# Performance work log

Measured on AMD Instinct MI355X. Metric: run time of the kernel, lower is better.

The kernel has to match this reference:

```python
import jax, jax.numpy as jnp
import numpy as np

QMIN, QMAX = -128.0, 127.0
SMALL_SCALE_THRESHOLD = 6.1e-05


def quant_kernel(x):
    # x: [M, K] float32 -> per-row scale (f32), zero point (i32), precomputed sum (i32), q (i8)
    rmin = jnp.minimum(jnp.min(x, axis=1), 0.0).astype(jnp.float32)
    rmax = jnp.maximum(jnp.max(x, axis=1), 0.0).astype(jnp.float32)
    scale = (rmax - rmin) / (QMAX - QMIN)
    # faithful replication of `scale == 0.0 + isinf(1/scale)` (precedence: 0.0 + bool)
    isinf = jnp.isinf(1.0 / scale)
    scale = jnp.where(scale == (0.0 + isinf.astype(jnp.float32)), 0.1, scale)
    small = scale < SMALL_SCALE_THRESHOLD
    amp = SMALL_SCALE_THRESHOLD / scale
    scale = jnp.where(small, SMALL_SCALE_THRESHOLD, scale)
    rmax = jnp.where(small, amp * rmax, rmax)
    rmin = jnp.where(small, amp * rmin, rmin)
    zp_from_min = QMIN - rmin / scale
    zp_from_max = QMAX - rmax / scale
    err_min = abs(QMIN) + jnp.abs(rmin / scale)
    err_max = abs(QMAX) + jnp.abs(rmax / scale)
    zp0 = jnp.where(err_min < err_max, zp_from_min, zp_from_max)
    zp = jnp.round(zp0).astype(jnp.int32)
    zp = jnp.where(zp0 < QMIN, jnp.int32(QMIN), zp)
    zp = jnp.where(zp0 > QMAX, jnp.int32(QMAX), zp)
    inv = 1.0 / scale
    sums = jnp.round(jnp.sum(x, axis=1) * inv).astype(jnp.int32)
    t = jnp.round(x * inv[:, None]) + zp[:, None].astype(jnp.float32)
    q = jnp.clip(t, QMIN, QMAX).astype(jnp.int8)
    return scale, zp, sums, q


def dequant_kernel(d, bias, m1_scales, m1_zeros, m1_sums, m2_scales, m2_zeros, m2_sums):
    # d: [M, N] int32 raw GEMM; m1_*: [M, 1]; m2_*: [1, N]
    temp = (m1_zeros * m2_sums).astype(jnp.int32) + (m1_sums * m2_zeros).astype(jnp.int32)
    scale = m1_scales * m2_scales
    return bias + ((d - temp).astype(jnp.float32) * scale).astype(bias.dtype)


def setup_inputs() -> dict:
    key = jax.random.key(0)
    k1, k2, k3, k4, k5 = jax.random.split(key, 5)
    B, S, K, N = 4, 4096, 1024, 1024
    inp = jax.random.normal(k1, (B, S, K), dtype=jnp.float32)
    qweight = jax.random.randint(k2, (N, K), -128, 128, dtype=jnp.int32).astype(jnp.int8)
    bias = jax.random.normal(k3, (N,), dtype=jnp.float32)
    w_scales = (jax.random.uniform(k4, (N,), dtype=jnp.float32) * 0.01 + 1e-3)
    w_zeros = jax.random.randint(k5, (N,), -10, 10, dtype=jnp.int32)
    # consistent precomputed weight sums (sum of quantized vals minus K*zero)
    w_sums = (jnp.sum(qweight.astype(jnp.int32), axis=1) - K * w_zeros).astype(jnp.int32)
    return {"inp": inp, "qweight": qweight, "bias": bias,
            "w_scales": w_scales, "w_zeros": w_zeros, "w_sums": w_sums}


def reference(inp, qweight, bias, w_scales, w_zeros, w_sums):
    B, S, K = inp.shape
    x = inp.reshape(B * S, K)
    scales, zeros, sums, qinp = quant_kernel(x)
    # int8 GEMM accumulated in int32: [M, K] @ [K, N]
    d = jnp.matmul(qinp.astype(jnp.int32), qweight.T.astype(jnp.int32))
    M, N = d.shape
    out = dequant_kernel(d, bias, scales.reshape(M, 1), zeros.reshape(M, 1),
                         sums.reshape(M, 1), w_scales.reshape(1, N),
                         w_zeros.reshape(1, N), w_sums.reshape(1, N))
    return out.reshape(B, S, N)
```

## Files before the change

### kernel.cpp

```cpp
#include <hip/hip_runtime.h>
#include <cstdint>
#include <cstddef>

typedef int v4i __attribute__((ext_vector_type(4)));

#define QMIN_F (-128.0f)
#define QMAX_F (127.0f)
#define SMALL_THR 6.1e-05f

#define WAITVM(n) asm volatile("s_waitcnt vmcnt(" #n ")" ::: "memory")
#define WAITLGKM0 asm volatile("s_waitcnt lgkmcnt(0)" ::: "memory")

__global__ __launch_bounds__(256) void quant_rows_kernel(
    const float* __restrict__ x, signed char* __restrict__ q,
    float* __restrict__ scales, int* __restrict__ zps, int* __restrict__ sums,
    const int* __restrict__ w32, int* __restrict__ w8pk, int n4, int K) {
  const int gidx = blockIdx.x * 256 + threadIdx.x;
  if (gidx < n4) {
    v4i pv = *(const v4i*)(w32 + gidx * 4);
    w8pk[gidx] = (pv.x & 255) | ((pv.y & 255) << 8) | ((pv.z & 255) << 16) |
                 (pv.w << 24);
  }

  const int wave = threadIdx.x >> 6;
  const int lane = threadIdx.x & 63;
  const int row  = blockIdx.x * 4 + wave;
  const float* xr = x + (size_t)row * K;

  float4 v[4];
  float vmin = 0.0f, vmax = 0.0f, vsum = 0.0f;
#pragma unroll
  for (int j = 0; j < 4; ++j) {
    v[j] = *(const float4*)(xr + j * 256 + lane * 4);
    vmin = fminf(vmin, fminf(fminf(v[j].x, v[j].y), fminf(v[j].z, v[j].w)));
    vmax = fmaxf(vmax, fmaxf(fmaxf(v[j].x, v[j].y), fmaxf(v[j].z, v[j].w)));
    vsum += (v[j].x + v[j].y) + (v[j].z + v[j].w);
  }
#pragma unroll
  for (int off = 32; off >= 1; off >>= 1) {
    vmin = fminf(vmin, __shfl_xor(vmin, off));
    vmax = fmaxf(vmax, __shfl_xor(vmax, off));
    vsum += __shfl_xor(vsum, off);
  }

  float scale = (vmax - vmin) / (QMAX_F - QMIN_F);
  float isinf_f = isinf(1.0f / scale) ? 1.0f : 0.0f;
  if (scale == isinf_f) scale = 0.1f;
  float rmin = vmin, rmax = vmax;
  if (scale < SMALL_THR) {
    float amp = SMALL_THR / scale;
    scale = SMALL_THR;
    rmax *= amp;
    rmin *= amp;
  }
  float rdmin = rmin / scale, rdmax = rmax / scale;
  float err_min = 128.0f + fabsf(rdmin);
  float err_max = 127.0f + fabsf(rdmax);
  float zp0 = (err_min < err_max) ? (QMIN_F - rdmin) : (QMAX_F - rdmax);
  int zp = (int)rintf(zp0);
  if (zp0 < QMIN_F) zp = -128;
  if (zp0 > QMAX_F) zp = 127;
  float inv = 1.0f / scale;

  if (lane == 0) {
    scales[row] = scale;
    zps[row]    = zp;
    sums[row]   = (int)rintf(vsum * inv);
  }

  const float zpf = (float)zp;
  int* qi = (int*)(q + (size_t)row * K);
#pragma unroll
  for (int j = 0; j < 4; ++j) {
    float t0 = fminf(fmaxf(rintf(v[j].x * inv) + zpf, QMIN_F), QMAX_F);
    float t1 = fminf(fmaxf(rintf(v[j].y * inv) + zpf, QMIN_F), QMAX_F);
    float t2 = fminf(fmaxf(rintf(v[j].z * inv) + zpf, QMIN_F), QMAX_F);
    float t3 = fminf(fmaxf(rintf(v[j].w * inv) + zpf, QMIN_F), QMAX_F);
    int pack = ((int)t0 & 255) | (((int)t1 & 255) << 8) |
               (((int)t2 & 255) << 16) | ((int)t3 << 24);
    qi[j * 64 + lane] = pack;
  }
}

__device__ __forceinline__ void gload_lds16(const void* g, void* l) {
  __builtin_amdgcn_global_load_lds(
      (const __attribute__((address_space(1))) void*)g,
      (__attribute__((address_space(3))) void*)l, 16, 0, 0);
}

__device__ __forceinline__ void stage_tile(
    const signed char* __restrict__ q, const signed char* __restrict__ w,
    char* buf, int rowA0, int rowB0, int k0, int K, int tid) {
#pragma unroll
  for (int i = 0; i < 2; ++i) {
    int c  = (i << 8) + tid;
    int r  = c >> 2;
    int sl = (c & 3) ^ ((r >> 1) & 3);
    gload_lds16(q + (size_t)(rowA0 + r) * K + k0 + (sl << 4), buf + (c << 4));
  }
#pragma unroll
  for (int i = 0; i < 2; ++i) {
    int c  = (i << 8) + tid;
    int r  = c >> 2;
    int sl = (c & 3) ^ ((r >> 1) & 3);
    gload_lds16(w + (size_t)(rowB0 + r) * K + k0 + (sl << 4),
                buf + 8192 + (c << 4));
  }
}

__global__ __launch_bounds__(256, 4) void gemm_dequant_kernel(
    const signed char* __restrict__ q, const signed char* __restrict__ w,
    const float* __restrict__ scales, const int* __restrict__ zps,
    const int* __restrict__ sums, const float* __restrict__ bias,
    const float* __restrict__ w_scales, const int* __restrict__ w_zeros,
    const int* __restrict__ w_sums, float* __restrict__ out,
    int N, int K, int nblk) {
  __shared__ char sh[2][16384];
  const int tid  = threadIdx.x;
  const int lane = tid & 63;
  const int wave = tid >> 6;
  const int wr = wave >> 1;
  const int wc = wave & 1;
  const int fr = lane & 15;
  const int kb = lane >> 4;
  const int ntN = N >> 7;
  const int per = nblk >> 3;
  const int lin = ((int)blockIdx.x & 7) * per + ((int)blockIdx.x >> 3);
  const int rowA0 = (lin / ntN) << 7;
  const int rowB0 = (lin % ntN) << 7;
  const int wrbase = wr << 6;
  const int wcbase = wc << 6;

  v4i acc[4][4];
#pragma unroll
  for (int i = 0; i < 4; ++i)
#pragma unroll
    for (int j = 0; j < 4; ++j) {
      v4i z = {0, 0, 0, 0};
      acc[i][j] = z;
    }

  const int NT = K >> 6;
  stage_tile(q, w, sh[0], rowA0, rowB0, 0, K, tid);

  for (int t = 0; t < NT; ++t) {
    if (t + 1 < NT) {
      stage_tile(q, w, sh[(t + 1) & 1], rowA0, rowB0, (t + 1) << 6, K, tid);
      WAITVM(4);
    } else {
      WAITVM(0);
    }
    __builtin_amdgcn_s_barrier();

    const char* bA = sh[t & 1];
    const char* bB = bA + 8192;

    v4i afrag[4], bfrag[4];
#pragma unroll
    for (int n = 0; n < 4; ++n) {
      int rb = wcbase + (n << 4) + fr;
      bfrag[n] = *(const v4i*)(bB + (rb << 6) + ((kb ^ ((rb >> 1) & 3)) << 4));
    }
#pragma unroll
    for (int m = 0; m < 4; ++m) {
      int ra = wrbase + (m << 4) + fr;
      afrag[m] = *(const v4i*)(bA + (ra << 6) + ((kb ^ ((ra >> 1) & 3)) << 4));
    }
    WAITLGKM0;
    __builtin_amdgcn_s_barrier();

    __builtin_amdgcn_s_setprio(1);
#pragma unroll
    for (int m = 0; m < 4; ++m)
#pragma unroll
      for (int n = 0; n < 4; ++n)
        acc[m][n] = __builtin_amdgcn_mfma_i32_16x16x64_i8(afrag[m], bfrag[n],
                                                          acc[m][n], 0, 0, 0);
    __builtin_amdgcn_s_setprio(0);
  }

  const int baseM = rowA0 + wrbase;
  const int baseN = rowB0 + wcbase;
  const int qr = (lane >> 4) << 2;
  const int qc = lane & 15;
  float cb[4], cwsc[4];
  int cwz[4], cws[4];
#pragma unroll
  for (int n = 0; n < 4; ++n) {
    int col = baseN + (n << 4) + qc;
    cb[n]   = bias[col];
    cwsc[n] = w_scales[col];
    cwz[n]  = w_zeros[col];
    cws[n]  = w_sums[col];
  }
#pragma unroll
  for (int i = 0; i < 4; ++i) {
    const int m0 = baseM + (i << 4) + qr;
    float sc[4];
    int zp4[4], sm4[4];
#pragma unroll
    for (int j = 0; j < 4; ++j) {
      sc[j]  = scales[m0 + j];
      zp4[j] = zps[m0 + j];
      sm4[j] = sums[m0 + j];
    }
#pragma unroll
    for (int n = 0; n < 4; ++n) {
      const int col = baseN + (n << 4) + qc;
#pragma unroll
      for (int j = 0; j < 4; ++j) {
        int d    = acc[i][n][j];
        int temp = zp4[j] * cws[n] + sm4[j] * cwz[n];
        out[(size_t)(m0 + j) * N + col] =
            cb[n] + (float)(d - temp) * (sc[j] * cwsc[n]);
      }
    }
  }
}

extern "C" void kernel_launch(void* const* d_in, const int* in_sizes, int n_in,
                              void* d_out, int out_size, void* d_ws, size_t ws_size,
                              hipStream_t stream) {
  const float* inp      = (const float*)d_in[0];
  const int*   qw32     = (const int*)d_in[1];
  const float* bias     = (const float*)d_in[2];
  const float* w_scales = (const float*)d_in[3];
  const int*   w_zeros  = (const int*)d_in[4];
  const int*   w_sums   = (const int*)d_in[5];

  const int N = in_sizes[2];
  const int K = in_sizes[1] / N;
  const int M = in_sizes[0] / K;

  float*       scales = (float*)d_ws;
  int*         zps    = (int*)((char*)d_ws + (size_t)M * 4);
  int*         sums   = (int*)((char*)d_ws + (size_t)M * 8);
  signed char* q      = (signed char*)((char*)d_ws + (size_t)M * 12);
  signed char* w8     = (signed char*)((char*)d_ws + (size_t)M * 12 + (size_t)M * K);

  const int n4 = (N * K) / 4;
  const int nblk = (M / 128) * (N / 128);
  quant_rows_kernel<<<M / 4, 256, 0, stream>>>(inp, q, scales, zps, sums,
                                               qw32, (int*)w8, n4, K);
  gemm_dequant_kernel<<<nblk, 256, 0, stream>>>(
      q, w8, scales, zps, sums, bias, w_scales, w_zeros, w_sums,
      (float*)d_out, N, K, nblk);
}
```

Before: 47.36 us.

## Persistent two-tile GEMM blocks with triple-buffered LDS and register double-buffered fragments

Each GEMM block now computes two 128x128 output tiles in sequence, so half as many blocks are launched. The K-loop uses three LDS stages and double-buffered register fragments, so LDS reads for the next step overlap the MFMA cluster of the current one. Staging continues across the tile boundary, and the first tile's epilogue runs mid-loop while the second tile's loads are in flight. In exchange, occupancy is lowered to 2 blocks per CU with more LDS and registers, and the tile count per block and K=1024 are hardcoded (32 stages).

```diff
diff --git a/kernel.cpp b/kernel.cpp
--- a/kernel.cpp
+++ b/kernel.cpp
@@ -10,6 +10,7 @@
 
 #define WAITVM(n) asm volatile("s_waitcnt vmcnt(" #n ")" ::: "memory")
 #define WAITLGKM0 asm volatile("s_waitcnt lgkmcnt(0)" ::: "memory")
+#define SCHEDBAR __builtin_amdgcn_sched_barrier(0)
 
 __global__ __launch_bounds__(256) void quant_rows_kernel(
     const float* __restrict__ x, signed char* __restrict__ q,
@@ -108,79 +109,40 @@
   }
 }
 
-__global__ __launch_bounds__(256, 4) void gemm_dequant_kernel(
-    const signed char* __restrict__ q, const signed char* __restrict__ w,
-    const float* __restrict__ scales, const int* __restrict__ zps,
-    const int* __restrict__ sums, const float* __restrict__ bias,
-    const float* __restrict__ w_scales, const int* __restrict__ w_zeros,
-    const int* __restrict__ w_sums, float* __restrict__ out,
-    int N, int K, int nblk) {
-  __shared__ char sh[2][16384];
-  const int tid  = threadIdx.x;
-  const int lane = tid & 63;
-  const int wave = tid >> 6;
-  const int wr = wave >> 1;
-  const int wc = wave & 1;
-  const int fr = lane & 15;
-  const int kb = lane >> 4;
-  const int ntN = N >> 7;
-  const int per = nblk >> 3;
-  const int lin = ((int)blockIdx.x & 7) * per + ((int)blockIdx.x >> 3);
-  const int rowA0 = (lin / ntN) << 7;
-  const int rowB0 = (lin % ntN) << 7;
-  const int wrbase = wr << 6;
-  const int wcbase = wc << 6;
-
-  v4i acc[4][4];
-#pragma unroll
-  for (int i = 0; i < 4; ++i)
-#pragma unroll
-    for (int j = 0; j < 4; ++j) {
-      v4i z = {0, 0, 0, 0};
-      acc[i][j] = z;
-    }
-
-  const int NT = K >> 6;
-  stage_tile(q, w, sh[0], rowA0, rowB0, 0, K, tid);
-
-  for (int t = 0; t < NT; ++t) {
-    if (t + 1 < NT) {
-      stage_tile(q, w, sh[(t + 1) & 1], rowA0, rowB0, (t + 1) << 6, K, tid);
-      WAITVM(4);
-    } else {
-      WAITVM(0);
-    }
-    __builtin_amdgcn_s_barrier();
-
-    const char* bA = sh[t & 1];
-    const char* bB = bA + 8192;
-
-    v4i afrag[4], bfrag[4];
-#pragma unroll
-    for (int n = 0; n < 4; ++n) {
-      int rb = wcbase + (n << 4) + fr;
-      bfrag[n] = *(const v4i*)(bB + (rb << 6) + ((kb ^ ((rb >> 1) & 3)) << 4));
-    }
-#pragma unroll
-    for (int m = 0; m < 4; ++m) {
-      int ra = wrbase + (m << 4) + fr;
-      afrag[m] = *(const v4i*)(bA + (ra << 6) + ((kb ^ ((ra >> 1) & 3)) << 4));
-    }
-    WAITLGKM0;
-    __builtin_amdgcn_s_barrier();
-
-    __builtin_amdgcn_s_setprio(1);
-#pragma unroll
-    for (int m = 0; m < 4; ++m)
-#pragma unroll
-      for (int n = 0; n < 4; ++n)
-        acc[m][n] = __builtin_amdgcn_mfma_i32_16x16x64_i8(afrag[m], bfrag[n],
-                                                          acc[m][n], 0, 0, 0);
-    __builtin_amdgcn_s_setprio(0);
-  }
-
-  const int baseM = rowA0 + wrbase;
-  const int baseN = rowB0 + wcbase;
+__device__ __forceinline__ void read_frags(const char* bA, v4i* af, v4i* bf,
+                                           int wrbase, int wcbase, int fr,
+                                           int kb) {
+  const char* bB = bA + 8192;
+#pragma unroll
+  for (int n = 0; n < 4; ++n) {
+    int rb = wcbase + (n << 4) + fr;
+    bf[n] = *(const v4i*)(bB + (rb << 6) + ((kb ^ ((rb >> 1) & 3)) << 4));
+  }
+#pragma unroll
+  for (int m = 0; m < 4; ++m) {
+    int ra = wrbase + (m << 4) + fr;
+    af[m] = *(const v4i*)(bA + (ra << 6) + ((kb ^ ((ra >> 1) & 3)) << 4));
+  }
+}
+
+__device__ __forceinline__ void mfma_cluster(v4i (&acc)[4][4], const v4i* af,
+                                             const v4i* bf) {
+  __builtin_amdgcn_s_setprio(1);
+#pragma unroll
+  for (int m = 0; m < 4; ++m)
+#pragma unroll
+    for (int n = 0; n < 4; ++n)
+      acc[m][n] = __builtin_amdgcn_mfma_i32_16x16x64_i8(af[m], bf[n],
+                                                        acc[m][n], 0, 0, 0);
+  __builtin_amdgcn_s_setprio(0);
+}
+
+__device__ __forceinline__ void epilogue_store(
+    v4i (&acc)[4][4], const float* __restrict__ scales,
+    const int* __restrict__ zps, const int* __restrict__ sums,
+    const float* __restrict__ bias, const float* __restrict__ w_scales,
+    const int* __restrict__ w_zeros, const int* __restrict__ w_sums,
+    float* __restrict__ out, int N, int baseM, int baseN, int lane) {
   const int qr = (lane >> 4) << 2;
   const int qc = lane & 15;
   float cb[4], cwsc[4];
@@ -216,6 +178,106 @@
       }
     }
   }
+}
+
+__global__ __launch_bounds__(256, 2) void gemm_dequant_kernel(
+    const signed char* __restrict__ q, const signed char* __restrict__ w,
+    const float* __restrict__ scales, const int* __restrict__ zps,
+    const int* __restrict__ sums, const float* __restrict__ bias,
+    const float* __restrict__ w_scales, const int* __restrict__ w_zeros,
+    const int* __restrict__ w_sums, float* __restrict__ out,
+    int N, int K, int ntiles) {
+  __shared__ char sh[3][16384];
+  const int tid  = threadIdx.x;
+  const int lane = tid & 63;
+  const int wave = tid >> 6;
+  const int wrbase = (wave >> 1) << 6;
+  const int wcbase = (wave & 1) << 6;
+  const int fr = lane & 15;
+  const int kb = lane >> 4;
+  const int ntN = N >> 7;
+  const int tpx  = ntiles >> 3;
+  const int half = tpx >> 1;
+  const int xcd  = (int)blockIdx.x & 7;
+  const int idx  = (int)blockIdx.x >> 3;
+  const int lin0 = xcd * tpx + idx;
+  const int lin1 = lin0 + half;
+  const int rowA0_0 = (lin0 / ntN) << 7, rowB0_0 = (lin0 % ntN) << 7;
+  const int rowA0_1 = (lin1 / ntN) << 7, rowB0_1 = (lin1 % ntN) << 7;
+
+#define STAGE(sidx, BUF)                                                \
+  do {                                                                  \
+    int _s = (sidx);                                                    \
+    if (_s < 32) {                                                      \
+      int _ra = (_s & 16) ? rowA0_1 : rowA0_0;                          \
+      int _rb = (_s & 16) ? rowB0_1 : rowB0_0;                          \
+      stage_tile(q, w, (BUF), _ra, _rb, (_s & 15) << 6, K, tid);        \
+    }                                                                   \
+  } while (0)
+
+  v4i acc[4][4];
+#pragma unroll
+  for (int i = 0; i < 4; ++i)
+#pragma unroll
+    for (int j = 0; j < 4; ++j) {
+      v4i z = {0, 0, 0, 0};
+      acc[i][j] = z;
+    }
+
+  char* P0 = sh[0];
+  char* P1 = sh[1];
+  char* P2 = sh[2];
+
+  v4i afA[4], bfA[4], afB[4], bfB[4];
+
+  STAGE(0, P0);
+  STAGE(1, P1);
+  WAITVM(4);
+  __builtin_amdgcn_s_barrier();
+  read_frags(P0, afA, bfA, wrbase, wcbase, fr, kb);
+  WAITLGKM0;
+  SCHEDBAR;
+
+  for (int tt = 0; tt < 32; tt += 2) {
+    STAGE(tt + 2, P2);
+    if (tt < 30) { WAITVM(4); } else { WAITVM(0); }
+    __builtin_amdgcn_s_barrier();
+    read_frags(P1, afB, bfB, wrbase, wcbase, fr, kb);
+    mfma_cluster(acc, afA, bfA);
+    WAITLGKM0;
+    SCHEDBAR;
+
+    STAGE(tt + 3, P0);
+    if (tt + 1 < 30) { WAITVM(4); } else { WAITVM(0); }
+    __builtin_amdgcn_s_barrier();
+    if (tt < 30) {
+      read_frags(P2, afA, bfA, wrbase, wcbase, fr, kb);
+    }
+    mfma_cluster(acc, afB, bfB);
+    WAITLGKM0;
+    SCHEDBAR;
+
+    char* tmp = P2;
+    P2 = P1;
+    P1 = P0;
+    P0 = tmp;
+
+    if (tt == 14) {
+      epilogue_store(acc, scales, zps, sums, bias, w_scales, w_zeros, w_sums,
+                     out, N, rowA0_0 + wrbase, rowB0_0 + wcbase, lane);
+#pragma unroll
+      for (int i = 0; i < 4; ++i)
+#pragma unroll
+        for (int j = 0; j < 4; ++j) {
+          v4i z = {0, 0, 0, 0};
+          acc[i][j] = z;
+        }
+    }
+  }
+
+  epilogue_store(acc, scales, zps, sums, bias, w_scales, w_zeros, w_sums,
+                 out, N, rowA0_1 + wrbase, rowB0_1 + wcbase, lane);
+#undef STAGE
 }
 
 extern "C" void kernel_launch(void* const* d_in, const int* in_sizes, int n_in,
@@ -239,10 +301,11 @@
   signed char* w8     = (signed char*)((char*)d_ws + (size_t)M * 12 + (size_t)M * K);
 
   const int n4 = (N * K) / 4;
-  const int nblk = (M / 128) * (N / 128);
+  const int ntiles = (M / 128) * (N / 128);
+  const int nblk   = ntiles / 2;
   quant_rows_kernel<<<M / 4, 256, 0, stream>>>(inp, q, scales, zps, sums,
                                                qw32, (int*)w8, n4, K);
   gemm_dequant_kernel<<<nblk, 256, 0, stream>>>(
       q, w8, scales, zps, sums, bias, w_scales, w_zeros, w_sums,
-      (float*)d_out, N, K, nblk);
-}
+      (float*)d_out, N, K, ntiles);
+}
```

New measurement: 48.15 us. No clear change (+1.7%).
